# Performance work log

Hardware: AMD Instinct MI355X
Metric: run time of the kernel (lower is better)

Reference implementation:

```python
import jax, jax.numpy as jnp
import numpy as np

N_NODES = 20000
DEG = 32
N_EDGES = N_NODES * DEG
NUM_USERS = 100000
D = 128


def setup_inputs() -> dict:
    key = jax.random.key(0)
    ks = jax.random.split(key, 10)
    nodes = jax.random.randint(ks[0], (N_NODES,), 0, NUM_USERS)
    neigh_idx = jax.random.randint(ks[1], (N_EDGES,), 0, NUM_USERS)
    # fixed-degree flattening of the ragged to_neighs lists: every node has DEG neighbors
    seg_ids = jnp.repeat(jnp.arange(N_NODES), DEG)
    u2e = jax.random.normal(ks[2], (NUM_USERS, D), dtype=jnp.float32)
    W1 = jax.random.normal(ks[3], (2 * D, D), dtype=jnp.float32) * 0.05
    b1 = jax.random.normal(ks[4], (D,), dtype=jnp.float32) * 0.05
    W2 = jax.random.normal(ks[5], (D, D), dtype=jnp.float32) * 0.05
    b2 = jax.random.normal(ks[6], (D,), dtype=jnp.float32) * 0.05
    w3 = jax.random.normal(ks[7], (D, 1), dtype=jnp.float32) * 0.05
    b3 = jax.random.normal(ks[8], (1,), dtype=jnp.float32) * 0.05
    return {"nodes": nodes, "neigh_idx": neigh_idx, "seg_ids": seg_ids,
            "u2e": u2e, "W1": W1, "b1": b1, "W2": W2, "b2": b2, "w3": w3, "b3": b3}


def reference(nodes, neigh_idx, seg_ids, u2e, W1, b1, W2, b2, w3, b3):
    n = nodes.shape[0]
    e_u = u2e[neigh_idx]                 # [E, D] neighbor embeddings
    u_rep = u2e[nodes][seg_ids]          # [E, D] center-node embedding repeated per neighbor
    x = jnp.concatenate([e_u, u_rep], axis=1)        # [E, 2D]
    h = jax.nn.relu(x @ W1 + b1)                      # [E, D]
    h = jax.nn.relu(h @ W2 + b2)                      # [E, D]
    s = (h @ w3 + b3)[:, 0]                           # [E] attention logits
    # segment softmax over each node's neighbor set
    smax = jax.ops.segment_max(s, seg_ids, num_segments=n)
    e = jnp.exp(s - smax[seg_ids])
    denom = jax.ops.segment_sum(e, seg_ids, num_segments=n)
    att = e / denom[seg_ids]                          # [E]
    # attention-weighted neighbor sum (e_u^T @ att per node)
    out = jax.ops.segment_sum(att[:, None] * e_u, seg_ids, num_segments=n)  # [N, D]
    return out
```

## Files before the change

### kernel.cpp

```cpp
#include <hip/hip_runtime.h>
#include <hip/hip_bf16.h>

#define DD 128
#define DEG 32

typedef __attribute__((ext_vector_type(8))) short short8;
typedef __attribute__((ext_vector_type(8))) _Float16 half8;
typedef __attribute__((ext_vector_type(4))) float f32x4;

__device__ __forceinline__ ushort f2bs(float x) {
    __hip_bfloat16 h = __float2bfloat16(x);
    return *reinterpret_cast<ushort*>(&h);
}
__device__ __forceinline__ float bs2f(ushort u) {
    return __uint_as_float(((unsigned)u) << 16);
}
__device__ __forceinline__ unsigned pack2(float a, float b) {
    return (unsigned)f2bs(a) | ((unsigned)f2bs(b) << 16);
}
__device__ __forceinline__ unsigned relu_add_pack(unsigned p, unsigned q) {
    float a0 = __uint_as_float(p << 16)        + __uint_as_float(q << 16);
    float a1 = __uint_as_float(p & 0xffff0000u) + __uint_as_float(q & 0xffff0000u);
    return pack2(fmaxf(a0, 0.f), fmaxf(a1, 0.f));
}

__global__ __launch_bounds__(256) void k_prep(
    const float* __restrict__ W1, const float* __restrict__ W2,
    uint4* __restrict__ w1img, uint4* __restrict__ w2t)
{
    int t = blockIdx.x * 256 + threadIdx.x;
    if (t < 4096) {
        int l = t & 63, f = t >> 6, k4 = f & 3, nt = f >> 2;
        int n = nt * 16 + (l & 15), kb = k4 * 32 + ((l >> 4) & 3) * 8;
        float v[8];
        #pragma unroll
        for (int i = 0; i < 8; ++i) {
            int k = kb + i;
            v[i] = (n < DD) ? W1[k * DD + n] : W1[(DD + k) * DD + (n - DD)];
        }
        uint4 r;
        r.x = pack2(v[0], v[1]); r.y = pack2(v[2], v[3]);
        r.z = pack2(v[4], v[5]); r.w = pack2(v[6], v[7]);
        w1img[t] = r;
    } else if (t < 6144) {
        int q = t - 4096;
        int l = q & 63, f = q >> 6, k4 = f & 3, mt = f >> 2;
        int ch = mt * 16 + (l & 15), kb = k4 * 32 + ((l >> 4) & 3) * 8;
        float v[8];
        #pragma unroll
        for (int i = 0; i < 8; ++i) v[i] = W2[(kb + i) * DD + ch];
        uint4 r;
        r.x = pack2(v[0], v[1]); r.y = pack2(v[2], v[3]);
        r.z = pack2(v[4], v[5]); r.w = pack2(v[6], v[7]);
        w2t[q] = r;
    }
}

__global__ __launch_bounds__(256) void k_pq(
    const float* __restrict__ u2e, const float* __restrict__ b1,
    const short8* __restrict__ w1img, ushort* __restrict__ Pb,
    ushort* __restrict__ Qb, _Float16* __restrict__ e16, int U)
{
    __shared__ __align__(16) char a_lds[128 * 256];
    const int t = threadIdx.x;
    const int w = t >> 6, l = t & 63;
    const int base = blockIdx.x * 128;

    #pragma unroll
    for (int i = 0; i < 8; ++i) {
        int flat = i * 256 + t;
        int row = flat >> 4, c8 = flat & 15;
        int grow = base + row;
        float4 v0 = make_float4(0, 0, 0, 0), v1 = v0;
        if (grow < U) {
            v0 = *reinterpret_cast<const float4*>(&u2e[(size_t)grow * DD + c8 * 8]);
            v1 = *reinterpret_cast<const float4*>(&u2e[(size_t)grow * DD + c8 * 8 + 4]);
        }
        if (grow < U) {
            half8 hv;
            hv[0] = (_Float16)v0.x; hv[1] = (_Float16)v0.y;
            hv[2] = (_Float16)v0.z; hv[3] = (_Float16)v0.w;
            hv[4] = (_Float16)v1.x; hv[5] = (_Float16)v1.y;
            hv[6] = (_Float16)v1.z; hv[7] = (_Float16)v1.w;
            *reinterpret_cast<half8*>(&e16[(size_t)grow * DD + c8 * 8]) = hv;
        }
        uint4 r;
        r.x = pack2(v0.x, v0.y); r.y = pack2(v0.z, v0.w);
        r.z = pack2(v1.x, v1.y); r.w = pack2(v1.z, v1.w);
        int off = (row * 256 + c8 * 16) ^ ((row & 7) << 4);
        *reinterpret_cast<uint4*>(a_lds + off) = r;
    }
    __syncthreads();

    short8 a[2][4];
    #pragma unroll
    for (int mt = 0; mt < 2; ++mt) {
        int row = w * 32 + mt * 16 + (l & 15);
        int sw = (row & 7) << 4;
        #pragma unroll
        for (int k4 = 0; k4 < 4; ++k4)
            a[mt][k4] = *reinterpret_cast<const short8*>(
                a_lds + ((row * 256 + k4 * 64 + (l >> 4) * 16) ^ sw));
    }

    const int chq = (l >> 4) << 2;
    #pragma unroll 2
    for (int mt = 0; mt < 8; ++mt) {
        short8 wf[4];
        #pragma unroll
        for (int k4 = 0; k4 < 4; ++k4) wf[k4] = w1img[(mt * 4 + k4) * 64 + l];
        #pragma unroll
        for (int ntu = 0; ntu < 2; ++ntu) {
            f32x4 acc = {0.f, 0.f, 0.f, 0.f};
            #pragma unroll
            for (int k4 = 0; k4 < 4; ++k4)
                acc = __builtin_amdgcn_mfma_f32_16x16x32_bf16(wf[k4], a[ntu][k4], acc, 0, 0, 0);
            int user = base + w * 32 + ntu * 16 + (l & 15);
            if (user < U) {
                uint2 pk;
                pk.x = pack2(acc[0], acc[1]); pk.y = pack2(acc[2], acc[3]);
                *reinterpret_cast<uint2*>(&Pb[(size_t)user * DD + mt * 16 + chq]) = pk;
            }
        }
    }
    #pragma unroll 2
    for (int mt = 8; mt < 16; ++mt) {
        short8 wf[4];
        #pragma unroll
        for (int k4 = 0; k4 < 4; ++k4) wf[k4] = w1img[(mt * 4 + k4) * 64 + l];
        float4 b1v = *reinterpret_cast<const float4*>(&b1[(mt - 8) * 16 + chq]);
        #pragma unroll
        for (int ntu = 0; ntu < 2; ++ntu) {
            f32x4 acc = {0.f, 0.f, 0.f, 0.f};
            #pragma unroll
            for (int k4 = 0; k4 < 4; ++k4)
                acc = __builtin_amdgcn_mfma_f32_16x16x32_bf16(wf[k4], a[ntu][k4], acc, 0, 0, 0);
            int user = base + w * 32 + ntu * 16 + (l & 15);
            if (user < U) {
                uint2 pk;
                pk.x = pack2(acc[0] + b1v.x, acc[1] + b1v.y);
                pk.y = pack2(acc[2] + b1v.z, acc[3] + b1v.w);
                *reinterpret_cast<uint2*>(&Qb[(size_t)user * DD + (mt - 8) * 16 + chq]) = pk;
            }
        }
    }
}

__global__ __launch_bounds__(256) void k_node(
    const int* __restrict__ nodes, const int* __restrict__ neigh,
    const _Float16* __restrict__ e16, const uint4* __restrict__ Pb4,
    const uint4* __restrict__ Qb4, const short8* __restrict__ w2t,
    const float* __restrict__ b2, const float* __restrict__ w3,
    float4* __restrict__ out4, int n)
{
    __shared__ __align__(16) char h_lds[128 * 256];
    __shared__ uint4 s_q16[4][16];
    __shared__ int   s_nb[128];
    __shared__ int   s_u[4];
    __shared__ float s_att[128];
    float* s_partf = reinterpret_cast<float*>(h_lds);

    const int t = threadIdx.x;
    const int w = t >> 6, l = t & 63;
    const int base = blockIdx.x * 4;

    if (t < 4)   s_u[t] = nodes[min(base + t, n - 1)];
    if (t < 128) s_nb[t] = neigh[min(base * DEG + t, n * DEG - 1)];
    __syncthreads();
    if (t < 64)  s_q16[t >> 4][t & 15] = Qb4[(size_t)s_u[t >> 4] * 16 + (t & 15)];
    __syncthreads();

    const int g4 = (t >> 4) & 3, c8 = t & 15, jg = t >> 6;
    half8 pre[8];
    #pragma unroll
    for (int j = 0; j < 8; ++j)
        pre[j] = *reinterpret_cast<const half8*>(
            &e16[(size_t)s_nb[g4 * DEG + jg * 8 + j] * DD + c8 * 8]);

    #pragma unroll
    for (int i = 0; i < 8; ++i) {
        int flat = i * 256 + t;
        int row = flat >> 4, cc = flat & 15;
        int nb = s_nb[row];
        uint4 pv = Pb4[(size_t)nb * 16 + cc];
        uint4 qv = s_q16[row >> 5][cc];
        uint4 r;
        r.x = relu_add_pack(pv.x, qv.x);
        r.y = relu_add_pack(pv.y, qv.y);
        r.z = relu_add_pack(pv.z, qv.z);
        r.w = relu_add_pack(pv.w, qv.w);
        int off = (row * 256 + cc * 16) ^ ((row & 7) << 4);
        *reinterpret_cast<uint4*>(h_lds + off) = r;
    }
    __syncthreads();

    short8 hb[2][4];
    #pragma unroll
    for (int nt = 0; nt < 2; ++nt) {
        int erow = w * 32 + nt * 16 + (l & 15);
        int sw = (erow & 7) << 4;
        #pragma unroll
        for (int k4 = 0; k4 < 4; ++k4)
            hb[nt][k4] = *reinterpret_cast<const short8*>(
                h_lds + ((erow * 256 + k4 * 64 + (l >> 4) * 16) ^ sw));
    }
    float pl0 = 0.f, pl1 = 0.f;
    #pragma unroll
    for (int mt = 0; mt < 8; ++mt) {
        short8 wf[4];
        #pragma unroll
        for (int k4 = 0; k4 < 4; ++k4) wf[k4] = w2t[(mt * 4 + k4) * 64 + l];
        float4 b2v = *reinterpret_cast<const float4*>(&b2[mt * 16 + (l >> 4) * 4]);
        float4 w3v = *reinterpret_cast<const float4*>(&w3[mt * 16 + (l >> 4) * 4]);
        f32x4 a0 = {0.f, 0.f, 0.f, 0.f}, a1 = {0.f, 0.f, 0.f, 0.f};
        #pragma unroll
        for (int k4 = 0; k4 < 4; ++k4)
            a0 = __builtin_amdgcn_mfma_f32_16x16x32_bf16(wf[k4], hb[0][k4], a0, 0, 0, 0);
        #pragma unroll
        for (int k4 = 0; k4 < 4; ++k4)
            a1 = __builtin_amdgcn_mfma_f32_16x16x32_bf16(wf[k4], hb[1][k4], a1, 0, 0, 0);
        pl0 += fmaxf(a0[0] + b2v.x, 0.f) * w3v.x + fmaxf(a0[1] + b2v.y, 0.f) * w3v.y
             + fmaxf(a0[2] + b2v.z, 0.f) * w3v.z + fmaxf(a0[3] + b2v.w, 0.f) * w3v.w;
        pl1 += fmaxf(a1[0] + b2v.x, 0.f) * w3v.x + fmaxf(a1[1] + b2v.y, 0.f) * w3v.y
             + fmaxf(a1[2] + b2v.z, 0.f) * w3v.z + fmaxf(a1[3] + b2v.w, 0.f) * w3v.w;
    }
    pl0 += __shfl_xor(pl0, 16); pl0 += __shfl_xor(pl0, 32);
    pl1 += __shfl_xor(pl1, 16); pl1 += __shfl_xor(pl1, 32);

    float mx = fmaxf(pl0, pl1);
    #pragma unroll
    for (int mask = 1; mask <= 8; mask <<= 1) mx = fmaxf(mx, __shfl_xor(mx, mask));
    float e0 = __expf(pl0 - mx), e1 = __expf(pl1 - mx);
    float sm = e0 + e1;
    #pragma unroll
    for (int mask = 1; mask <= 8; mask <<= 1) sm += __shfl_xor(sm, mask);
    if (l < 16) {
        float inv = __frcp_rn(sm);
        s_att[w * DEG + l]      = e0 * inv;
        s_att[w * DEG + 16 + l] = e1 * inv;
    }
    __syncthreads();

    float o[8] = {0.f, 0.f, 0.f, 0.f, 0.f, 0.f, 0.f, 0.f};
    #pragma unroll
    for (int j = 0; j < 8; ++j) {
        float a = s_att[g4 * DEG + jg * 8 + j];
        #pragma unroll
        for (int i = 0; i < 8; ++i)
            o[i] = fmaf(a, (float)pre[j][i], o[i]);
    }
    {
        float* sp = s_partf + ((jg * 4 + g4) * 128 + c8 * 8);
        #pragma unroll
        for (int i = 0; i < 8; ++i) sp[i] = o[i];
    }
    __syncthreads();
    if (t < 128) {
        int g = t >> 5, c4 = t & 31;
        float4 r = make_float4(0.f, 0.f, 0.f, 0.f);
        #pragma unroll
        for (int j2 = 0; j2 < 4; ++j2) {
            const float* sp = s_partf + ((j2 * 4 + g) * 128 + c4 * 4);
            r.x += sp[0]; r.y += sp[1]; r.z += sp[2]; r.w += sp[3];
        }
        if (base + g < n) out4[(size_t)(base + g) * 32 + c4] = r;
    }
}

extern "C" void kernel_launch(void* const* d_in, const int* in_sizes, int n_in,
                              void* d_out, int out_size, void* d_ws, size_t ws_size,
                              hipStream_t stream)
{
    const int*   nodes = (const int*)  d_in[0];
    const int*   neigh = (const int*)  d_in[1];
    const float* u2e   = (const float*)d_in[3];
    const float* W1    = (const float*)d_in[4];
    const float* b1    = (const float*)d_in[5];
    const float* W2    = (const float*)d_in[6];
    const float* b2    = (const float*)d_in[7];
    const float* w3    = (const float*)d_in[8];

    const int n = in_sizes[0];
    const int U = in_sizes[3] / DD;

    uint4*     w1img = (uint4*)d_ws;
    uint4*     w2t   = w1img + 4096;
    ushort*    Pb    = (ushort*)(w2t + 2048);
    ushort*    Qb    = Pb + (size_t)U * DD;
    _Float16*  e16   = (_Float16*)(Qb + (size_t)U * DD);

    k_prep<<<24, 256, 0, stream>>>(W1, W2, w1img, w2t);
    k_pq<<<(U + 127) / 128, 256, 0, stream>>>(u2e, b1, (const short8*)w1img,
                                              Pb, Qb, e16, U);
    k_node<<<(n + 3) / 4, 256, 0, stream>>>(nodes, neigh, e16,
                                            (const uint4*)Pb, (const uint4*)Qb,
                                            (const short8*)w2t, b2, w3,
                                            (float4*)d_out, n);
}
```

Baseline: 118.6 us.

## Load MFMA operands directly from global memory, removing LDS staging in both kernels

In k_pq and k_node, each lane now loads its MFMA operand fragments straight from global memory (u2e rows, and the Pb/Qb rows with the relu-add applied in registers) instead of staging tiles through swizzled shared memory. This removes 32 KB of LDS per block and several __syncthreads barriers, which should raise occupancy and cut latency. The trade-off is less coalesced 32-byte-per-lane global accesses, and in k_node Qb and the neighbor indices are read redundantly by each lane. The shared partial-sum buffer is now a separate array and the accumulation uses float4 stores.

```diff
diff --git a/kernel.cpp b/kernel.cpp
--- a/kernel.cpp
+++ b/kernel.cpp
@@ -11,9 +11,6 @@
 __device__ __forceinline__ ushort f2bs(float x) {
     __hip_bfloat16 h = __float2bfloat16(x);
     return *reinterpret_cast<ushort*>(&h);
-}
-__device__ __forceinline__ float bs2f(ushort u) {
-    return __uint_as_float(((unsigned)u) << 16);
 }
 __device__ __forceinline__ unsigned pack2(float a, float b) {
     return (unsigned)f2bs(a) | ((unsigned)f2bs(b) << 16);
@@ -61,46 +58,34 @@
     const short8* __restrict__ w1img, ushort* __restrict__ Pb,
     ushort* __restrict__ Qb, _Float16* __restrict__ e16, int U)
 {
-    __shared__ __align__(16) char a_lds[128 * 256];
     const int t = threadIdx.x;
     const int w = t >> 6, l = t & 63;
     const int base = blockIdx.x * 128;
 
-    #pragma unroll
-    for (int i = 0; i < 8; ++i) {
-        int flat = i * 256 + t;
-        int row = flat >> 4, c8 = flat & 15;
-        int grow = base + row;
-        float4 v0 = make_float4(0, 0, 0, 0), v1 = v0;
-        if (grow < U) {
-            v0 = *reinterpret_cast<const float4*>(&u2e[(size_t)grow * DD + c8 * 8]);
-            v1 = *reinterpret_cast<const float4*>(&u2e[(size_t)grow * DD + c8 * 8 + 4]);
-        }
-        if (grow < U) {
-            half8 hv;
-            hv[0] = (_Float16)v0.x; hv[1] = (_Float16)v0.y;
-            hv[2] = (_Float16)v0.z; hv[3] = (_Float16)v0.w;
-            hv[4] = (_Float16)v1.x; hv[5] = (_Float16)v1.y;
-            hv[6] = (_Float16)v1.z; hv[7] = (_Float16)v1.w;
-            *reinterpret_cast<half8*>(&e16[(size_t)grow * DD + c8 * 8]) = hv;
-        }
-        uint4 r;
-        r.x = pack2(v0.x, v0.y); r.y = pack2(v0.z, v0.w);
-        r.z = pack2(v1.x, v1.y); r.w = pack2(v1.z, v1.w);
-        int off = (row * 256 + c8 * 16) ^ ((row & 7) << 4);
-        *reinterpret_cast<uint4*>(a_lds + off) = r;
-    }
-    __syncthreads();
-
     short8 a[2][4];
     #pragma unroll
     for (int mt = 0; mt < 2; ++mt) {
-        int row = w * 32 + mt * 16 + (l & 15);
-        int sw = (row & 7) << 4;
-        #pragma unroll
-        for (int k4 = 0; k4 < 4; ++k4)
-            a[mt][k4] = *reinterpret_cast<const short8*>(
-                a_lds + ((row * 256 + k4 * 64 + (l >> 4) * 16) ^ sw));
+        int user = base + w * 32 + mt * 16 + (l & 15);
+        int ruser = min(user, U - 1);
+        const float* rp = u2e + (size_t)ruser * DD + ((l >> 4) << 3);
+        #pragma unroll
+        for (int k4 = 0; k4 < 4; ++k4) {
+            float4 v0 = *reinterpret_cast<const float4*>(rp + k4 * 32);
+            float4 v1 = *reinterpret_cast<const float4*>(rp + k4 * 32 + 4);
+            uint4 r;
+            r.x = pack2(v0.x, v0.y); r.y = pack2(v0.z, v0.w);
+            r.z = pack2(v1.x, v1.y); r.w = pack2(v1.z, v1.w);
+            a[mt][k4] = *reinterpret_cast<short8*>(&r);
+            if (user < U) {
+                half8 hv;
+                hv[0] = (_Float16)v0.x; hv[1] = (_Float16)v0.y;
+                hv[2] = (_Float16)v0.z; hv[3] = (_Float16)v0.w;
+                hv[4] = (_Float16)v1.x; hv[5] = (_Float16)v1.y;
+                hv[6] = (_Float16)v1.z; hv[7] = (_Float16)v1.w;
+                *reinterpret_cast<half8*>(
+                    &e16[(size_t)user * DD + k4 * 32 + ((l >> 4) << 3)]) = hv;
+            }
+        }
     }
 
     const int chq = (l >> 4) << 2;
@@ -148,62 +133,50 @@
 
 __global__ __launch_bounds__(256) void k_node(
     const int* __restrict__ nodes, const int* __restrict__ neigh,
-    const _Float16* __restrict__ e16, const uint4* __restrict__ Pb4,
-    const uint4* __restrict__ Qb4, const short8* __restrict__ w2t,
+    const _Float16* __restrict__ e16, const ushort* __restrict__ Pb,
+    const ushort* __restrict__ Qb, const short8* __restrict__ w2t,
     const float* __restrict__ b2, const float* __restrict__ w3,
     float4* __restrict__ out4, int n)
 {
-    __shared__ __align__(16) char h_lds[128 * 256];
-    __shared__ uint4 s_q16[4][16];
-    __shared__ int   s_nb[128];
-    __shared__ int   s_u[4];
     __shared__ float s_att[128];
-    float* s_partf = reinterpret_cast<float*>(h_lds);
+    __shared__ float s_part[16 * 128];
 
     const int t = threadIdx.x;
     const int w = t >> 6, l = t & 63;
     const int base = blockIdx.x * 4;
-
-    if (t < 4)   s_u[t] = nodes[min(base + t, n - 1)];
-    if (t < 128) s_nb[t] = neigh[min(base * DEG + t, n * DEG - 1)];
-    __syncthreads();
-    if (t < 64)  s_q16[t >> 4][t & 15] = Qb4[(size_t)s_u[t >> 4] * 16 + (t & 15)];
-    __syncthreads();
-
-    const int g4 = (t >> 4) & 3, c8 = t & 15, jg = t >> 6;
+    const int node = base + w;
+
+    const int g4 = (t >> 4) & 3, c8 = t & 15;
     half8 pre[8];
     #pragma unroll
-    for (int j = 0; j < 8; ++j)
-        pre[j] = *reinterpret_cast<const half8*>(
-            &e16[(size_t)s_nb[g4 * DEG + jg * 8 + j] * DD + c8 * 8]);
-
-    #pragma unroll
-    for (int i = 0; i < 8; ++i) {
-        int flat = i * 256 + t;
-        int row = flat >> 4, cc = flat & 15;
-        int nb = s_nb[row];
-        uint4 pv = Pb4[(size_t)nb * 16 + cc];
-        uint4 qv = s_q16[row >> 5][cc];
-        uint4 r;
-        r.x = relu_add_pack(pv.x, qv.x);
-        r.y = relu_add_pack(pv.y, qv.y);
-        r.z = relu_add_pack(pv.z, qv.z);
-        r.w = relu_add_pack(pv.w, qv.w);
-        int off = (row * 256 + cc * 16) ^ ((row & 7) << 4);
-        *reinterpret_cast<uint4*>(h_lds + off) = r;
-    }
-    __syncthreads();
-
+    for (int j = 0; j < 8; ++j) {
+        int nb = neigh[(base + g4) * DEG + w * 8 + j];
+        pre[j] = *reinterpret_cast<const half8*>(&e16[(size_t)nb * DD + c8 * 8]);
+    }
+
+    const int u = nodes[node];
+    const int koff = ((l >> 4) << 3);
+    uint4 qv[4];
+    #pragma unroll
+    for (int k4 = 0; k4 < 4; ++k4)
+        qv[k4] = *reinterpret_cast<const uint4*>(&Qb[(size_t)u * DD + k4 * 32 + koff]);
     short8 hb[2][4];
     #pragma unroll
     for (int nt = 0; nt < 2; ++nt) {
-        int erow = w * 32 + nt * 16 + (l & 15);
-        int sw = (erow & 7) << 4;
-        #pragma unroll
-        for (int k4 = 0; k4 < 4; ++k4)
-            hb[nt][k4] = *reinterpret_cast<const short8*>(
-                h_lds + ((erow * 256 + k4 * 64 + (l >> 4) * 16) ^ sw));
-    }
+        int nb = neigh[node * DEG + nt * 16 + (l & 15)];
+        const ushort* prow = Pb + (size_t)nb * DD + koff;
+        #pragma unroll
+        for (int k4 = 0; k4 < 4; ++k4) {
+            uint4 pv = *reinterpret_cast<const uint4*>(prow + k4 * 32);
+            uint4 r;
+            r.x = relu_add_pack(pv.x, qv[k4].x);
+            r.y = relu_add_pack(pv.y, qv[k4].y);
+            r.z = relu_add_pack(pv.z, qv[k4].z);
+            r.w = relu_add_pack(pv.w, qv[k4].w);
+            hb[nt][k4] = *reinterpret_cast<short8*>(&r);
+        }
+    }
+
     float pl0 = 0.f, pl1 = 0.f;
     #pragma unroll
     for (int mt = 0; mt < 8; ++mt) {
@@ -241,18 +214,18 @@
     }
     __syncthreads();
 
-    float o[8] = {0.f, 0.f, 0.f, 0.f, 0.f, 0.f, 0.f, 0.f};
+    float4 oa = make_float4(0.f, 0.f, 0.f, 0.f), ob = oa;
     #pragma unroll
     for (int j = 0; j < 8; ++j) {
-        float a = s_att[g4 * DEG + jg * 8 + j];
-        #pragma unroll
-        for (int i = 0; i < 8; ++i)
-            o[i] = fmaf(a, (float)pre[j][i], o[i]);
+        float a = s_att[g4 * DEG + w * 8 + j];
+        oa.x = fmaf(a, (float)pre[j][0], oa.x); oa.y = fmaf(a, (float)pre[j][1], oa.y);
+        oa.z = fmaf(a, (float)pre[j][2], oa.z); oa.w = fmaf(a, (float)pre[j][3], oa.w);
+        ob.x = fmaf(a, (float)pre[j][4], ob.x); ob.y = fmaf(a, (float)pre[j][5], ob.y);
+        ob.z = fmaf(a, (float)pre[j][6], ob.z); ob.w = fmaf(a, (float)pre[j][7], ob.w);
     }
     {
-        float* sp = s_partf + ((jg * 4 + g4) * 128 + c8 * 8);
-        #pragma unroll
-        for (int i = 0; i < 8; ++i) sp[i] = o[i];
+        float4* sp = reinterpret_cast<float4*>(s_part + ((w * 4 + g4) * 128 + c8 * 8));
+        sp[0] = oa; sp[1] = ob;
     }
     __syncthreads();
     if (t < 128) {
@@ -260,7 +233,7 @@
         float4 r = make_float4(0.f, 0.f, 0.f, 0.f);
         #pragma unroll
         for (int j2 = 0; j2 < 4; ++j2) {
-            const float* sp = s_partf + ((j2 * 4 + g) * 128 + c4 * 4);
+            const float* sp = s_part + ((j2 * 4 + g) * 128 + c4 * 4);
             r.x += sp[0]; r.y += sp[1]; r.z += sp[2]; r.w += sp[3];
         }
         if (base + g < n) out4[(size_t)(base + g) * 32 + c4] = r;
@@ -293,7 +266,7 @@
     k_pq<<<(U + 127) / 128, 256, 0, stream>>>(u2e, b1, (const short8*)w1img,
                                               Pb, Qb, e16, U);
     k_node<<<(n + 3) / 4, 256, 0, stream>>>(nodes, neigh, e16,
-                                            (const uint4*)Pb, (const uint4*)Qb,
+                                            Pb, Qb,
                                             (const short8*)w2t, b2, w3,
                                             (float4*)d_out, n);
 }
```

Result: slower. 122.7 us (+3.5%).
